# Performance work log

Measured on AMD Instinct MI355X. Metric: run time of the kernel, lower is better.

Reference implementation:

```python
import jax, jax.numpy as jnp
import numpy as np

NEG_INF = -9e16
SLOPE = 0.2  # leaky relu slope


def setup_inputs() -> dict:
    key = jax.random.key(0)
    k1, k2, k3, k4 = jax.random.split(key, 4)
    N, F_in, H, D = 3072, 512, 8, 64
    h = jax.random.normal(k1, (N, F_in), dtype=jnp.float32)
    adj = jax.random.randint(k2, (N, N), 0, 2, dtype=jnp.int32)
    W = jax.random.normal(k3, (H, F_in, D), dtype=jnp.float32) * (2.0 / (F_in + D)) ** 0.5
    a = jax.random.normal(k4, (H, 2 * D, 1), dtype=jnp.float32) * (2.0 / (2 * D + 1)) ** 0.5
    return {"h": h, "adj": adj, "W": W, "a": a}


def reference(h, adj, W, a):
    # h: [N, F], W: [H, F, D], a: [H, 2D, 1], adj: [N, N]
    H, _, D = W.shape
    ht = jnp.einsum("nf,hfd->hnd", h, W)            # [H, N, D]
    a_src = a[:, :D, 0]                               # [H, D]
    a_dst = a[:, D:, 0]                               # [H, D]
    src = jnp.einsum("hnd,hd->hn", ht, a_src)        # [H, N]
    dst = jnp.einsum("hnd,hd->hn", ht, a_dst)        # [H, N]
    e = src[:, :, None] + dst[:, None, :]             # [H, N, N]
    e = jnp.where(e > 0, e, SLOPE * e)                # leaky relu
    e = jnp.where(adj[None] > 0, e, NEG_INF)
    att = jax.nn.softmax(e, axis=-1)                  # [H, N, N]
    hp = jnp.einsum("hnm,hmd->hnd", att, ht)         # [H, N, D]
    out = jnp.transpose(hp, (1, 0, 2)).reshape(h.shape[0], H * D)  # concat heads
    return (out, att)
```

## Files before the change

### kernel.cpp

```cpp
#include <hip/hip_runtime.h>

#define NN 3072
#define FF 512
#define HH 8
#define DD 64
#define SLOPEV 0.2f
#define CH2 64
#define NC2 (NN/CH2)

typedef __bf16  bf16x8 __attribute__((ext_vector_type(8)));
typedef __bf16  bf16x4 __attribute__((ext_vector_type(4)));
typedef short   s16x8  __attribute__((ext_vector_type(8)));
typedef float   f32x4  __attribute__((ext_vector_type(4)));
typedef unsigned long long u64;

#define MFMA16(a,b,c) __builtin_amdgcn_mfma_f32_16x16x32_bf16((a),(b),(c),0,0,0)

__device__ __forceinline__ short f2bf(float x){ __bf16 b=(__bf16)x; return __builtin_bit_cast(short,b); }
__device__ __forceinline__ float bf2f(short s){ return (float)__builtin_bit_cast(__bf16,s); }
__device__ __forceinline__ bf16x8 ldbf8(const short* p){ return __builtin_bit_cast(bf16x8, *(const s16x8*)p); }

__device__ __forceinline__ void gload16(const void* g, void* l){
  __builtin_amdgcn_global_load_lds(
      (const __attribute__((address_space(1))) void*)(uintptr_t)g,
      (__attribute__((address_space(3))) void*)(uint32_t)(uintptr_t)l, 16, 0, 0);
}

__global__ __launch_bounds__(256) void k_split_h(const float* __restrict__ h,
    short* __restrict__ hhi, short* __restrict__ hlo){
  size_t base = ((size_t)blockIdx.x*256 + threadIdx.x)*8;
  float4 v0 = *(const float4*)(h+base);
  float4 v1 = *(const float4*)(h+base+4);
  float vv[8] = {v0.x,v0.y,v0.z,v0.w,v1.x,v1.y,v1.z,v1.w};
  s16x8 hi, lo;
  #pragma unroll
  for (int j=0;j<8;j++){ short s=f2bf(vv[j]); hi[j]=s; lo[j]=f2bf(vv[j]-bf2f(s)); }
  *(s16x8*)(hhi+base)=hi; *(s16x8*)(hlo+base)=lo;
}

__global__ __launch_bounds__(64) void k_wt(const float* __restrict__ W, const float* __restrict__ a,
    short* __restrict__ wthi, short* __restrict__ wtlo,
    float* __restrict__ wasrc, float* __restrict__ wadst){
  int h = blockIdx.y, f0 = blockIdx.x*8, d = threadIdx.x;
  float asv = a[h*2*DD + d];
  float adv = a[h*2*DD + DD + d];
  s16x8 vh, vl;
  #pragma unroll
  for (int j=0;j<8;j++){
    float v = W[((size_t)h*FF + f0 + j)*DD + d];
    short s = f2bf(v); vh[j]=s; vl[j]=f2bf(v-bf2f(s));
    float ws_ = v*asv, wd_ = v*adv;
    #pragma unroll
    for (int m=1;m<64;m<<=1){ ws_ += __shfl_xor(ws_,m,64); wd_ += __shfl_xor(wd_,m,64); }
    if (d==0){ wasrc[h*FF+f0+j]=ws_; wadst[h*FF+f0+j]=wd_; }
  }
  size_t o = ((size_t)h*DD + d)*FF + f0;
  *(s16x8*)(wthi+o)=vh; *(s16x8*)(wtlo+o)=vl;
}

__global__ __launch_bounds__(256) void k_pack(const int* __restrict__ adj, u64* __restrict__ padj){
  int idx = blockIdx.x*256 + threadIdx.x;
  u64 b = __ballot(adj[idx] > 0);
  if ((threadIdx.x & 63) == 0) padj[idx>>6] = b;
}

__global__ __launch_bounds__(256) void k_srcdst(const float* __restrict__ h,
    const float* __restrict__ wasrc, const float* __restrict__ wadst,
    float* __restrict__ src, float* __restrict__ dst){
  int n = blockIdx.x*4 + (threadIdx.x>>6);
  int lane = threadIdx.x & 63;
  const float* hp = h + (size_t)n*FF + lane*8;
  float4 x0 = *(const float4*)hp, x1 = *(const float4*)(hp+4);
  float xs[8] = {x0.x,x0.y,x0.z,x0.w,x1.x,x1.y,x1.z,x1.w};
  float ps[HH], pd[HH];
  #pragma unroll
  for (int hh=0; hh<HH; hh++){
    const float* sp = wasrc + (size_t)hh*FF + lane*8;
    const float* dp = wadst + (size_t)hh*FF + lane*8;
    float4 s0 = *(const float4*)sp, s1 = *(const float4*)(sp+4);
    float4 t0 = *(const float4*)dp, t1 = *(const float4*)(dp+4);
    ps[hh] = xs[0]*s0.x + xs[1]*s0.y + xs[2]*s0.z + xs[3]*s0.w
           + xs[4]*s1.x + xs[5]*s1.y + xs[6]*s1.z + xs[7]*s1.w;
    pd[hh] = xs[0]*t0.x + xs[1]*t0.y + xs[2]*t0.z + xs[3]*t0.w
           + xs[4]*t1.x + xs[5]*t1.y + xs[6]*t1.z + xs[7]*t1.w;
  }
  #pragma unroll
  for (int m=1;m<64;m<<=1){
    #pragma unroll
    for (int hh=0; hh<HH; hh++){ ps[hh] += __shfl_xor(ps[hh],m,64); pd[hh] += __shfl_xor(pd[hh],m,64); }
  }
  if (lane==0){
    #pragma unroll
    for (int hh=0; hh<HH; hh++){ src[hh*NN+n]=ps[hh]; dst[hh*NN+n]=pd[hh]; }
  }
}

__global__ __launch_bounds__(128) void k_ht(const short* __restrict__ hhi, const short* __restrict__ hlo,
    const short* __restrict__ wthi, const short* __restrict__ wtlo,
    short* __restrict__ hthi, short* __restrict__ htlo){
  int h = blockIdx.y, n0 = blockIdx.x*32;
  int w = threadIdx.x>>6, lane = threadIdx.x&63;
  int r15 = lane&15, g = lane>>4;
  int arow = n0 + w*16 + r15;
  f32x4 acc[4] = {{0.f,0.f,0.f,0.f},{0.f,0.f,0.f,0.f},{0.f,0.f,0.f,0.f},{0.f,0.f,0.f,0.f}};
  const short* ha = hhi + (size_t)arow*FF + g*8;
  const short* la = hlo + (size_t)arow*FF + g*8;
  for (int kk=0; kk<FF; kk+=32){
    bf16x8 ahi = ldbf8(ha+kk), alo = ldbf8(la+kk);
    #pragma unroll
    for (int c=0;c<4;c++){
      size_t bo = ((size_t)h*DD + c*16 + r15)*FF + g*8 + kk;
      bf16x8 bh = ldbf8(wthi + bo), bl = ldbf8(wtlo + bo);
      acc[c] = MFMA16(ahi,bh,acc[c]);
      acc[c] = MFMA16(ahi,bl,acc[c]);
      acc[c] = MFMA16(alo,bh,acc[c]);
    }
  }
  #pragma unroll
  for (int c=0;c<4;c++){
    #pragma unroll
    for (int r=0;r<4;r++){
      float v = acc[c][r];
      short s = f2bf(v); short sl = f2bf(v - bf2f(s));
      int n = n0 + w*16 + g*4 + r;
      size_t o = ((size_t)h*DD + c*16 + r15)*NN + n;
      hthi[o]=s; htlo[o]=sl;
    }
  }
}

__global__ __launch_bounds__(512, 8) void k_att(const u64* __restrict__ padj,
    const float* __restrict__ src, const float* __restrict__ dst,
    const short* __restrict__ hthi, const short* __restrict__ htlo,
    float* __restrict__ dout){
  __shared__ short hA[64][CH2], lA[64][CH2], hB[64][CH2], lB[64][CH2];
  __shared__ short pA[32][CH2], pB[32][CH2];
  const size_t OUTOFF = (size_t)NN*HH*DD;
  int bid = blockIdx.x;
  int h = bid & 7, n0 = (bid >> 3) * 32;
  int t = threadIdx.x;
  int r = t>>4, j = t&15;
  int nrow = n0 + r;
  float srcv = src[h*NN + nrow];
  const float* dsth = dst + h*NN;
  const u64* arow = padj + (size_t)nrow*(NN/64);

  int wv = t>>6, lane = t&63, r15 = lane&15, g = lane>>4;
  int cblk = wv&3, nh = wv>>2;
  int drow = t>>3;
  int sslot = (t&7) ^ (drow&7);
  const short* gh = hthi + ((size_t)(h*DD) + drow)*NN + sslot*8;
  const short* gl = htlo + ((size_t)(h*DD) + drow)*NN + sslot*8;

  gload16(gh, &hA[wv*8][0]);
  gload16(gl, &lA[wv*8][0]);

  float psum = 0.f;
  for (int c=0;c<24;c++){
    u64 w0 = arow[c*2], w1 = arow[c*2+1];
    const float* dp = dsth + c*128 + j*4;
    float4 d0 = *(const float4*)dp, d1 = *(const float4*)(dp+64);
    float dj[8] = {d0.x,d0.y,d0.z,d0.w,d1.x,d1.y,d1.z,d1.w};
    #pragma unroll
    for (int e=0;e<8;e++){
      float ev = srcv + dj[e];
      ev = fmaxf(ev, SLOPEV*ev);
      u64 bits = (e<4) ? w0 : w1;
      float p = ((bits >> (j*4 + (e&3))) & 1ull) ? __expf(ev) : 0.f;
      psum += p;
    }
  }
  #pragma unroll
  for (int m=1;m<16;m<<=1) psum += __shfl_xor(psum, m, 64);
  float inv = (psum > 0.f) ? 1.f/psum : (1.f/(float)NN);
  bool am = !(psum > 0.f);

  f32x4 acc = {0.f,0.f,0.f,0.f};
  float* attrow = dout + OUTOFF + ((size_t)(h*NN + nrow))*NN;
  int aoff0 = (cblk*16 + r15)*(CH2*2);
  int boff0 = (nh*16 + r15)*(CH2*2);
  int csw   = (r15&7)<<4;
  int pofs  = r*(CH2*2) + ((j*8) ^ ((r&7)<<4));

  u64 bits = arow[0];
  const float* dvp = dsth + j*4;
  float4 dv = *(const float4*)dvp;

  #pragma unroll 2
  for (int c=0;c<NC2-1;c++){
    short (*hc)[CH2]; short (*lc)[CH2]; short (*hn)[CH2]; short (*ln)[CH2]; short (*pc)[CH2];
    if (c&1){ hc=hB; lc=lB; hn=hA; ln=lA; pc=pB; }
    else    { hc=hA; lc=lA; hn=hB; ln=lB; pc=pA; }

    gload16(gh + (c+1)*CH2, &hn[wv*8][0]);
    gload16(gl + (c+1)*CH2, &ln[wv*8][0]);
    u64 bits_n = arow[c+1];
    float4 dv_n = *(const float4*)(dvp + (c+1)*CH2);
    float o[4];
    #pragma unroll
    for (int e=0;e<4;e++){
      float ev = srcv + ((const float*)&dv)[e];
      ev = fmaxf(ev, SLOPEV*ev);
      float p = ((bits >> (j*4 + e)) & 1ull) ? __expf(ev) : 0.f;
      if (am) p = 1.f;
      o[e] = p * inv;
    }
    f32x4 s0 = {o[0],o[1],o[2],o[3]};
    __builtin_nontemporal_store(s0, (f32x4*)(attrow + c*CH2 + j*4));
    bf16x4 pb;
    #pragma unroll
    for (int e=0;e<4;e++) pb[e] = (__bf16)o[e];
    *(bf16x4*)((char*)pc + pofs) = pb;

    __builtin_amdgcn_sched_barrier(0);
    asm volatile("s_waitcnt vmcnt(5) lgkmcnt(0)" ::: "memory");
    __builtin_amdgcn_sched_barrier(0);
    __builtin_amdgcn_s_barrier();
    __builtin_amdgcn_sched_barrier(0);

    const char* hcB = (const char*)hc;
    const char* lcB = (const char*)lc;
    const char* pcB = (const char*)pc;
    #pragma unroll
    for (int ks=0;ks<2;ks++){
      int kb = (g*16 + ks*64) ^ csw;
      bf16x8 bf = *(const bf16x8*)(pcB + boff0 + kb);
      bf16x8 ah = *(const bf16x8*)(hcB + aoff0 + kb);
      bf16x8 al = *(const bf16x8*)(lcB + aoff0 + kb);
      acc = MFMA16(ah, bf, acc);
      acc = MFMA16(al, bf, acc);
    }
    asm volatile("" ::: "memory");
    __builtin_amdgcn_s_barrier();
    __builtin_amdgcn_sched_barrier(0);

    bits = bits_n; dv = dv_n;
  }

  {
    const int c = NC2-1;
    short (*hc)[CH2] = (c&1)?hB:hA; short (*lc)[CH2] = (c&1)?lB:lA;
    short (*pc)[CH2] = (c&1)?pB:pA;
    float o[4];
    #pragma unroll
    for (int e=0;e<4;e++){
      float ev = srcv + ((const float*)&dv)[e];
      ev = fmaxf(ev, SLOPEV*ev);
      float p = ((bits >> (j*4 + e)) & 1ull) ? __expf(ev) : 0.f;
      if (am) p = 1.f;
      o[e] = p * inv;
    }
    f32x4 s0 = {o[0],o[1],o[2],o[3]};
    __builtin_nontemporal_store(s0, (f32x4*)(attrow + c*CH2 + j*4));
    bf16x4 pb;
    #pragma unroll
    for (int e=0;e<4;e++) pb[e] = (__bf16)o[e];
    *(bf16x4*)((char*)pc + pofs) = pb;

    __builtin_amdgcn_sched_barrier(0);
    asm volatile("s_waitcnt vmcnt(1) lgkmcnt(0)" ::: "memory");
    __builtin_amdgcn_sched_barrier(0);
    __builtin_amdgcn_s_barrier();
    __builtin_amdgcn_sched_barrier(0);

    const char* hcB = (const char*)hc;
    const char* lcB = (const char*)lc;
    const char* pcB = (const char*)pc;
    #pragma unroll
    for (int ks=0;ks<2;ks++){
      int kb = (g*16 + ks*64) ^ csw;
      bf16x8 bf = *(const bf16x8*)(pcB + boff0 + kb);
      bf16x8 ah = *(const bf16x8*)(hcB + aoff0 + kb);
      bf16x8 al = *(const bf16x8*)(lcB + aoff0 + kb);
      acc = MFMA16(ah, bf, acc);
      acc = MFMA16(al, bf, acc);
    }
  }

  int n = n0 + nh*16 + r15;
  size_t ob = (size_t)n*(HH*DD) + h*DD + cblk*16 + g*4;
  __builtin_nontemporal_store(acc, (f32x4*)(dout+ob));
}

extern "C" void kernel_launch(void* const* d_in, const int* in_sizes, int n_in,
                              void* d_out, int out_size, void* d_ws, size_t ws_size,
                              hipStream_t stream) {
  const float* h   = (const float*)d_in[0];
  const int*   adj = (const int*)d_in[1];
  const float* W   = (const float*)d_in[2];
  const float* a   = (const float*)d_in[3];
  float* out = (float*)d_out;

  short* hhi  = (short*)d_ws;
  short* hlo  = hhi  + (size_t)NN*FF;
  short* wthi = hlo  + (size_t)NN*FF;
  short* wtlo = wthi + (size_t)HH*DD*FF;
  short* hthi = wtlo + (size_t)HH*DD*FF;
  short* htlo = hthi + (size_t)HH*DD*NN;
  float* wasrc= (float*)(htlo + (size_t)HH*DD*NN);
  float* wadst= wasrc + HH*FF;
  float* srcb = wadst + HH*FF;
  float* dstb = srcb + HH*NN;
  u64*   padj = (u64*)(dstb + HH*NN);

  k_split_h<<<dim3(NN*FF/(256*8)), 256, 0, stream>>>(h, hhi, hlo);
  k_wt     <<<dim3(FF/8, HH), 64, 0, stream>>>(W, a, wthi, wtlo, wasrc, wadst);
  k_pack   <<<dim3(NN*NN/256), 256, 0, stream>>>(adj, padj);
  k_srcdst <<<dim3(NN/4), 256, 0, stream>>>(h, wasrc, wadst, srcb, dstb);
  k_ht     <<<dim3(NN/32, HH), 128, 0, stream>>>(hhi, hlo, wthi, wtlo, hthi, htlo);
  k_att    <<<dim3(NN/32*HH), 512, 0, stream>>>(padj, srcb, dstb, hthi, htlo, out);
}
```

Measured before the change: 153.7 us.

## Drop bf16 lo-split of ht, precompute softmax row sums in separate kernel

Stores ht as a single bf16 plane instead of a hi/lo pair. This halves the LDS tiles, global loads and MFMAs in the attention-times-values loop, but loosens accuracy on the aggregated output. The softmax denominator pass moves out of k_att into a new k_rowsum kernel with one wave per row. The ht epilogue now stages through LDS so global writes are coalesced 16-byte stores. Together these shorten the main attention kernel at the cost of an extra launch and a second read of the adjacency bits.

```diff
diff --git a/kernel.cpp b/kernel.cpp
--- a/kernel.cpp
+++ b/kernel.cpp
@@ -95,9 +95,33 @@
   }
 }
 
+__global__ __launch_bounds__(256) void k_rowsum(const u64* __restrict__ padj,
+    const float* __restrict__ src, const float* __restrict__ dst,
+    float* __restrict__ rowsums){
+  int wid = blockIdx.x*4 + (threadIdx.x>>6);
+  int lane = threadIdx.x & 63;
+  int h = wid / NN, n = wid - h*NN;
+  float srcv = src[h*NN + n];
+  const float* dsth = dst + h*NN;
+  const u64* arow = padj + (size_t)n*(NN/64);
+  float s = 0.f;
+  #pragma unroll 4
+  for (int i=0;i<NN/64;i++){
+    u64 w = arow[i];
+    float dv = dsth[i*64 + lane];
+    float ev = srcv + dv;
+    ev = fmaxf(ev, SLOPEV*ev);
+    s += ((w >> lane) & 1ull) ? __expf(ev) : 0.f;
+  }
+  #pragma unroll
+  for (int m=1;m<64;m<<=1) s += __shfl_xor(s, m, 64);
+  if (lane == 0) rowsums[h*NN + n] = s;
+}
+
 __global__ __launch_bounds__(128) void k_ht(const short* __restrict__ hhi, const short* __restrict__ hlo,
     const short* __restrict__ wthi, const short* __restrict__ wtlo,
-    short* __restrict__ hthi, short* __restrict__ htlo){
+    short* __restrict__ hthi){
+  __shared__ short tH[64][40];
   int h = blockIdx.y, n0 = blockIdx.x*32;
   int w = threadIdx.x>>6, lane = threadIdx.x&63;
   int r15 = lane&15, g = lane>>4;
@@ -120,20 +144,22 @@
   for (int c=0;c<4;c++){
     #pragma unroll
     for (int r=0;r<4;r++){
-      float v = acc[c][r];
-      short s = f2bf(v); short sl = f2bf(v - bf2f(s));
-      int n = n0 + w*16 + g*4 + r;
-      size_t o = ((size_t)h*DD + c*16 + r15)*NN + n;
-      hthi[o]=s; htlo[o]=sl;
-    }
-  }
+      int dloc = c*16 + r15, nloc = w*16 + g*4 + r;
+      tH[dloc][nloc] = f2bf(acc[c][r]);
+    }
+  }
+  __syncthreads();
+  int row = threadIdx.x>>1, half = threadIdx.x&1;
+  size_t o = ((size_t)h*DD + row)*NN + n0 + half*16;
+  *(s16x8*)(hthi + o)     = *(const s16x8*)&tH[row][half*16];
+  *(s16x8*)(hthi + o + 8) = *(const s16x8*)&tH[row][half*16+8];
 }
 
 __global__ __launch_bounds__(512, 8) void k_att(const u64* __restrict__ padj,
     const float* __restrict__ src, const float* __restrict__ dst,
-    const short* __restrict__ hthi, const short* __restrict__ htlo,
-    float* __restrict__ dout){
-  __shared__ short hA[64][CH2], lA[64][CH2], hB[64][CH2], lB[64][CH2];
+    const float* __restrict__ rowsums,
+    const short* __restrict__ hthi, float* __restrict__ dout){
+  __shared__ short hA[64][CH2], hB[64][CH2];
   __shared__ short pA[32][CH2], pB[32][CH2];
   const size_t OUTOFF = (size_t)NN*HH*DD;
   int bid = blockIdx.x;
@@ -150,30 +176,12 @@
   int drow = t>>3;
   int sslot = (t&7) ^ (drow&7);
   const short* gh = hthi + ((size_t)(h*DD) + drow)*NN + sslot*8;
-  const short* gl = htlo + ((size_t)(h*DD) + drow)*NN + sslot*8;
 
   gload16(gh, &hA[wv*8][0]);
-  gload16(gl, &lA[wv*8][0]);
-
-  float psum = 0.f;
-  for (int c=0;c<24;c++){
-    u64 w0 = arow[c*2], w1 = arow[c*2+1];
-    const float* dp = dsth + c*128 + j*4;
-    float4 d0 = *(const float4*)dp, d1 = *(const float4*)(dp+64);
-    float dj[8] = {d0.x,d0.y,d0.z,d0.w,d1.x,d1.y,d1.z,d1.w};
-    #pragma unroll
-    for (int e=0;e<8;e++){
-      float ev = srcv + dj[e];
-      ev = fmaxf(ev, SLOPEV*ev);
-      u64 bits = (e<4) ? w0 : w1;
-      float p = ((bits >> (j*4 + (e&3))) & 1ull) ? __expf(ev) : 0.f;
-      psum += p;
-    }
-  }
-  #pragma unroll
-  for (int m=1;m<16;m<<=1) psum += __shfl_xor(psum, m, 64);
-  float inv = (psum > 0.f) ? 1.f/psum : (1.f/(float)NN);
-  bool am = !(psum > 0.f);
+
+  float tot = rowsums[h*NN + nrow];
+  float inv = (tot > 0.f) ? 1.f/tot : (1.f/(float)NN);
+  bool am = !(tot > 0.f);
 
   f32x4 acc = {0.f,0.f,0.f,0.f};
   float* attrow = dout + OUTOFF + ((size_t)(h*NN + nrow))*NN;
@@ -188,12 +196,11 @@
 
   #pragma unroll 2
   for (int c=0;c<NC2-1;c++){
-    short (*hc)[CH2]; short (*lc)[CH2]; short (*hn)[CH2]; short (*ln)[CH2]; short (*pc)[CH2];
-    if (c&1){ hc=hB; lc=lB; hn=hA; ln=lA; pc=pB; }
-    else    { hc=hA; lc=lA; hn=hB; ln=lB; pc=pA; }
+    short (*hc)[CH2] = (c&1)?hB:hA;
+    short (*hn)[CH2] = (c&1)?hA:hB;
+    short (*pc)[CH2] = (c&1)?pB:pA;
 
     gload16(gh + (c+1)*CH2, &hn[wv*8][0]);
-    gload16(gl + (c+1)*CH2, &ln[wv*8][0]);
     u64 bits_n = arow[c+1];
     float4 dv_n = *(const float4*)(dvp + (c+1)*CH2);
     float o[4];
@@ -213,22 +220,19 @@
     *(bf16x4*)((char*)pc + pofs) = pb;
 
     __builtin_amdgcn_sched_barrier(0);
-    asm volatile("s_waitcnt vmcnt(5) lgkmcnt(0)" ::: "memory");
+    asm volatile("s_waitcnt vmcnt(4) lgkmcnt(0)" ::: "memory");
     __builtin_amdgcn_sched_barrier(0);
     __builtin_amdgcn_s_barrier();
     __builtin_amdgcn_sched_barrier(0);
 
     const char* hcB = (const char*)hc;
-    const char* lcB = (const char*)lc;
     const char* pcB = (const char*)pc;
     #pragma unroll
     for (int ks=0;ks<2;ks++){
       int kb = (g*16 + ks*64) ^ csw;
       bf16x8 bf = *(const bf16x8*)(pcB + boff0 + kb);
       bf16x8 ah = *(const bf16x8*)(hcB + aoff0 + kb);
-      bf16x8 al = *(const bf16x8*)(lcB + aoff0 + kb);
       acc = MFMA16(ah, bf, acc);
-      acc = MFMA16(al, bf, acc);
     }
     asm volatile("" ::: "memory");
     __builtin_amdgcn_s_barrier();
@@ -239,7 +243,7 @@
 
   {
     const int c = NC2-1;
-    short (*hc)[CH2] = (c&1)?hB:hA; short (*lc)[CH2] = (c&1)?lB:lA;
+    short (*hc)[CH2] = (c&1)?hB:hA;
     short (*pc)[CH2] = (c&1)?pB:pA;
     float o[4];
     #pragma unroll
@@ -258,22 +262,19 @@
     *(bf16x4*)((char*)pc + pofs) = pb;
 
     __builtin_amdgcn_sched_barrier(0);
-    asm volatile("s_waitcnt vmcnt(1) lgkmcnt(0)" ::: "memory");
+    asm volatile("s_waitcnt vmcnt(4) lgkmcnt(0)" ::: "memory");
     __builtin_amdgcn_sched_barrier(0);
     __builtin_amdgcn_s_barrier();
     __builtin_amdgcn_sched_barrier(0);
 
     const char* hcB = (const char*)hc;
-    const char* lcB = (const char*)lc;
     const char* pcB = (const char*)pc;
     #pragma unroll
     for (int ks=0;ks<2;ks++){
       int kb = (g*16 + ks*64) ^ csw;
       bf16x8 bf = *(const bf16x8*)(pcB + boff0 + kb);
       bf16x8 ah = *(const bf16x8*)(hcB + aoff0 + kb);
-      bf16x8 al = *(const bf16x8*)(lcB + aoff0 + kb);
       acc = MFMA16(ah, bf, acc);
-      acc = MFMA16(al, bf, acc);
     }
   }
 
@@ -296,17 +297,18 @@
   short* wthi = hlo  + (size_t)NN*FF;
   short* wtlo = wthi + (size_t)HH*DD*FF;
   short* hthi = wtlo + (size_t)HH*DD*FF;
-  short* htlo = hthi + (size_t)HH*DD*NN;
-  float* wasrc= (float*)(htlo + (size_t)HH*DD*NN);
+  float* wasrc= (float*)(hthi + (size_t)HH*DD*NN);
   float* wadst= wasrc + HH*FF;
   float* srcb = wadst + HH*FF;
   float* dstb = srcb + HH*NN;
-  u64*   padj = (u64*)(dstb + HH*NN);
+  float* rsum = dstb + HH*NN;
+  u64*   padj = (u64*)(rsum + HH*NN);
 
   k_split_h<<<dim3(NN*FF/(256*8)), 256, 0, stream>>>(h, hhi, hlo);
   k_wt     <<<dim3(FF/8, HH), 64, 0, stream>>>(W, a, wthi, wtlo, wasrc, wadst);
   k_pack   <<<dim3(NN*NN/256), 256, 0, stream>>>(adj, padj);
   k_srcdst <<<dim3(NN/4), 256, 0, stream>>>(h, wasrc, wadst, srcb, dstb);
-  k_ht     <<<dim3(NN/32, HH), 128, 0, stream>>>(hhi, hlo, wthi, wtlo, hthi, htlo);
-  k_att    <<<dim3(NN/32*HH), 512, 0, stream>>>(padj, srcb, dstb, hthi, htlo, out);
-}
+  k_ht     <<<dim3(NN/32, HH), 128, 0, stream>>>(hhi, hlo, wthi, wtlo, hthi);
+  k_rowsum <<<dim3(HH*NN/4), 256, 0, stream>>>(padj, srcb, dstb, rsum);
+  k_att    <<<dim3(NN/32*HH), 512, 0, stream>>>(padj, srcb, dstb, rsum, hthi, out);
+}
```

Result: slower. 161.6 us (+5.2%).
